# Kernel optimization log

Hardware: AMD Instinct MI355X
Metric: run time of the kernel (lower is better)

The kernel has to match this reference:

```python
import jax, jax.numpy as jnp
import numpy as np

B, S, HID = 1, 2048, 4096
H, HKV = 32, 8
D = HID // H          # 128
G = H // HKV          # 4 query heads per kv head (GQA)


def setup_inputs() -> dict:
    key = jax.random.key(0)
    ks = jax.random.split(key, 5)
    hidden_states = jax.random.normal(ks[0], (B, S, HID), dtype=jnp.float32)
    # additive causal mask: 0 on/below diagonal, large negative above
    causal = jnp.tril(jnp.ones((S, S), dtype=bool))
    attention_mask = jnp.where(causal, 0.0, -1e9).astype(jnp.float32)[None, None]
    sc = 0.02
    wq = jax.random.normal(ks[1], (HID, H * D), dtype=jnp.float32) * sc
    wk = jax.random.normal(ks[2], (HID, HKV * D), dtype=jnp.float32) * sc
    wv = jax.random.normal(ks[3], (HID, HKV * D), dtype=jnp.float32) * sc
    wo = jax.random.normal(ks[4], (H * D, HID), dtype=jnp.float32) * sc
    return {"hidden_states": hidden_states, "attention_mask": attention_mask,
            "wq": wq, "wk": wk, "wv": wv, "wo": wo}


def reference(hidden_states, attention_mask, wq, wk, wv, wo):
    # projections (lora_rank=0 path: plain dense, no bias)
    q = hidden_states @ wq                      # [B,S,H*D]
    k = hidden_states @ wk                      # [B,S,HKV*D]
    v = hidden_states @ wv                      # [B,S,HKV*D]
    # split heads; group query heads by their kv head: head h -> (h//G, h%G)
    q = q.reshape(B, S, HKV, G, D).transpose(0, 2, 3, 1, 4)   # [B,HKV,G,S,D]
    k = k.reshape(B, S, HKV, D).transpose(0, 2, 1, 3)          # [B,HKV,S,D]
    v = v.reshape(B, S, HKV, D).transpose(0, 2, 1, 3)          # [B,HKV,S,D]
    scale = 1.0 / jnp.sqrt(jnp.float32(D))
    # explicit S x S scores (as in source), with GQA kv broadcast over G
    scores = jnp.einsum('bkgsd,bktd->bkgst', q, k) * scale     # [B,HKV,G,S,S]
    scores = scores + attention_mask[:, :, None]               # broadcast over G
    probs = jax.nn.softmax(scores, axis=-1)
    attn = jnp.einsum('bkgst,bktd->bkgsd', probs, v)           # [B,HKV,G,S,D]
    attn = attn.transpose(0, 3, 1, 2, 4).reshape(B, S, H * D)  # [B,S,H*D]
    return attn @ wo                                           # [B,S,HID]
```

## Files before the change

kernel.cpp:

```cpp
#include <hip/hip_runtime.h>
#include <hip/hip_bf16.h>

#define S_LEN 2048
#define HID 4096
#define NH 32
#define NKV 8
#define HD 128
#define LDQKV 6144

typedef __bf16 bf16x8 __attribute__((ext_vector_type(8)));
typedef __bf16 bf16x4 __attribute__((ext_vector_type(4)));
typedef float f32x4 __attribute__((ext_vector_type(4)));

#define GLD16(gp, lp)                                                                   \
    __builtin_amdgcn_global_load_lds((const __attribute__((address_space(1))) void*)(gp), \
                                     (__attribute__((address_space(3))) void*)(lp), 16, 0, 0)

#define MFMA_BF16(a, b, c) __builtin_amdgcn_mfma_f32_16x16x32_bf16((a), (b), (c), 0, 0, 0)

__global__ void cast_bf16_kernel(const float* __restrict__ x, __bf16* __restrict__ y, int n) {
    int i = (blockIdx.x * blockDim.x + threadIdx.x) * 4;
    if (i < n) {
        float4 v = *reinterpret_cast<const float4*>(x + i);
        bf16x4 o;
        o.x = (__bf16)v.x; o.y = (__bf16)v.y; o.z = (__bf16)v.z; o.w = (__bf16)v.w;
        *reinterpret_cast<bf16x4*>(y + i) = o;
    }
}

__global__ void transpose_cast_kernel(const float* __restrict__ W, __bf16* __restrict__ WT,
                                      int K, int N, float scale) {
    __shared__ float tile[32][33];
    int bx = blockIdx.x;
    int by = blockIdx.y;
    int tx = threadIdx.x;
    int ty = threadIdx.y;
    int n = bx * 32 + tx;
#pragma unroll
    for (int i = 0; i < 4; i++) {
        int k = by * 32 + ty + i * 8;
        tile[ty + i * 8][tx] = W[(size_t)k * N + n];
    }
    __syncthreads();
    int k2 = by * 32 + tx;
#pragma unroll
    for (int i = 0; i < 4; i++) {
        int n2 = bx * 32 + ty + i * 8;
        WT[(size_t)n2 * K + k2] = (__bf16)(tile[tx][ty + i * 8] * scale);
    }
}

__global__ void transpose_bf16_kernel(const __bf16* __restrict__ V, int ldin,
                                      __bf16* __restrict__ VT, int ldout) {
    __shared__ __bf16 tile[32][33];
    int bx = blockIdx.x;
    int by = blockIdx.y;
    int tx = threadIdx.x;
    int ty = threadIdx.y;
#pragma unroll
    for (int i = 0; i < 4; i++)
        tile[ty + i * 8][tx] = V[(size_t)(by * 32 + ty + i * 8) * ldin + bx * 32 + tx];
    __syncthreads();
#pragma unroll
    for (int i = 0; i < 4; i++)
        VT[(size_t)(bx * 32 + ty + i * 8) * ldout + by * 32 + tx] = tile[tx][ty + i * 8];
}

template <int BM, typename OUT_T>
__global__ __launch_bounds__(512, 1) void gemm_pipe_kernel(const __bf16* __restrict__ A, int lda,
                                                           const __bf16* __restrict__ BT, int ldb,
                                                           OUT_T* __restrict__ C, int ldc, int K) {
    constexpr int MR = BM / 128;
    constexpr int AROUNDS = BM / 64;
    constexpr int NREADS = 4 * MR + 4;
    __shared__ __bf16 As[2][BM * 64];
    __shared__ __bf16 Bs[2][256 * 64];
    const int n0 = blockIdx.x * 256;
    const int m0 = blockIdx.y * BM;
    const int tid = threadIdx.x;
    const int lane = tid & 63, quad = lane >> 4, l16 = lane & 15;
    const int wave = tid >> 6;
    const int wg = (wave >> 2) * 64;
    const int wn32 = (wave & 3) * 32;

    f32x4 acc[4 * MR][4] = {};

    auto STAGE = [&](int b, int kb) {
#pragma unroll
        for (int r = 0; r < AROUNDS; r++) {
            int c = r * 512 + tid;
            int row = c >> 3;
            int col8 = (c & 7) ^ (row & 7);
            GLD16(&A[(size_t)(m0 + row) * lda + kb + col8 * 8], &As[b][c * 8]);
        }
#pragma unroll
        for (int r = 0; r < 4; r++) {
            int c = r * 512 + tid;
            int row = c >> 3;
            int col8 = (c & 7) ^ (row & 7);
            GLD16(&BT[(size_t)(n0 + row) * ldb + kb + col8 * 8], &Bs[b][c * 8]);
        }
    };

    auto READ_SET = [&](const __bf16* Asb, const __bf16* Bsb, int kk,
                        bf16x8 (&fa)[4 * MR], bf16x8 (&fb)[4]) {
        int slot = ((kk * 4 + quad) ^ (l16 & 7)) * 8;
#pragma unroll
        for (int i = 0; i < 4 * MR; i++) {
            int row = wg + (i & 3) * 16 + (i >> 2) * 128 + l16;
            fa[i] = *reinterpret_cast<const bf16x8*>(&Asb[row * 64 + slot]);
        }
#pragma unroll
        for (int j = 0; j < 4; j++) {
            int row = wn32 + (j & 1) * 16 + (j >> 1) * 128 + l16;
            fb[j] = *reinterpret_cast<const bf16x8*>(&Bsb[row * 64 + slot]);
        }
    };

    auto MF = [&](bf16x8 (&fa)[4 * MR], bf16x8 (&fb)[4]) {
        __builtin_amdgcn_s_setprio(1);
#pragma unroll
        for (int i = 0; i < 4 * MR; i++)
#pragma unroll
            for (int j = 0; j < 4; j++)
                acc[i][j] = MFMA_BF16(fa[i], fb[j], acc[i][j]);
        __builtin_amdgcn_s_setprio(0);
    };

    auto WAIT_SET = [&]() {
        if constexpr (NREADS == 12) {
            asm volatile("s_waitcnt lgkmcnt(12)" ::: "memory");
        } else {
            asm volatile("s_waitcnt lgkmcnt(8)" ::: "memory");
        }
        __builtin_amdgcn_sched_barrier(0);
    };

    const int nk = K >> 6;
    bf16x8 fa0[4 * MR], fb0[4], fa1[4 * MR], fb1[4];

    STAGE(0, 0);
    STAGE(1, 64);
    if constexpr (AROUNDS == 4) {
        asm volatile("s_waitcnt vmcnt(8)" ::: "memory");
    } else {
        asm volatile("s_waitcnt vmcnt(6)" ::: "memory");
    }
    __builtin_amdgcn_sched_barrier(0);
    __builtin_amdgcn_s_barrier();
    READ_SET(As[0], Bs[0], 0, fa0, fb0);

    for (int kt = 0; kt < nk; ++kt) {
        const int cur = kt & 1;
        READ_SET(As[cur], Bs[cur], 1, fa1, fb1);
        WAIT_SET();
        MF(fa0, fb0);
        if (kt + 1 < nk) {
            asm volatile("s_waitcnt vmcnt(0)" ::: "memory");
            __builtin_amdgcn_sched_barrier(0);
            __builtin_amdgcn_s_barrier();
            READ_SET(As[cur ^ 1], Bs[cur ^ 1], 0, fa0, fb0);
            WAIT_SET();
        } else {
            asm volatile("s_waitcnt lgkmcnt(0)" ::: "memory");
            __builtin_amdgcn_sched_barrier(0);
        }
        if (kt + 2 < nk) {
            __builtin_amdgcn_s_barrier();
            STAGE(cur, (kt + 2) << 6);
        }
        MF(fa1, fb1);
    }

#pragma unroll
    for (int i = 0; i < 4 * MR; i++)
#pragma unroll
        for (int j = 0; j < 4; j++)
#pragma unroll
            for (int r = 0; r < 4; r++) {
                int row = m0 + wg + (i & 3) * 16 + (i >> 2) * 128 + quad * 4 + r;
                int col = n0 + wn32 + (j & 1) * 16 + (j >> 1) * 128 + l16;
                C[(size_t)row * ldc + col] = (OUT_T)acc[i][j][r];
            }
}

__global__ __launch_bounds__(256) void attn_kernel(const __bf16* __restrict__ QKV,
                                                   const __bf16* __restrict__ VT,
                                                   __bf16* __restrict__ Ao,
                                                   __bf16* __restrict__ Opart,
                                                   float* __restrict__ Lp) {
    __shared__ __bf16 Ks[64 * 128];
    __shared__ __bf16 Vs[128 * 64];
    __shared__ __bf16 Pl[4][2][16 * 72];
    int x = blockIdx.x;
    int qt, c;
    if (x < 32) { qt = 31 - (x >> 1); c = x & 1; }
    else        { qt = 47 - x;        c = 0;     }
    int hp = blockIdx.y;
    int kvh = hp >> 1;
    int h0 = kvh * 4 + (hp & 1) * 2;
    int t0 = c ? 16 : 0;
    int t1 = c ? qt : min(qt, 15);
    int tid = threadIdx.x;
    int wave = tid >> 6, lane = tid & 63, quad = lane >> 4, l16 = lane & 15;
    int wq = qt * 64 + wave * 16;
    const __bf16* Kb = QKV + HID + (size_t)kvh * HD;
    const __bf16* Vt = VT + (size_t)kvh * HD * S_LEN;

    bf16x8 qf[2][4];
#pragma unroll
    for (int h = 0; h < 2; h++)
#pragma unroll
        for (int ks = 0; ks < 4; ks++)
            qf[h][ks] = *reinterpret_cast<const bf16x8*>(
                &QKV[(size_t)(wq + l16) * LDQKV + (h0 + h) * HD + ks * 32 + quad * 8]);

    bf16x8 ones;
#pragma unroll
    for (int j = 0; j < 8; j++) ones[j] = (__bf16)1.0f;

    f32x4 acc_o[2][8] = {};
    f32x4 lacc[2] = {};

    for (int t = t0; t <= t1; t++) {
        int kv0 = t << 6;
        bool diag = (t == qt);
        __syncthreads();
#pragma unroll
        for (int i = 0; i < 4; i++) {
            int cc = i * 256 + tid;
            int row = cc >> 4, sub = cc & 15;
            int col8 = sub ^ (row & 15);
            GLD16(&Kb[(size_t)(kv0 + row) * LDQKV + col8 * 8], &Ks[cc * 8]);
        }
#pragma unroll
        for (int i = 0; i < 4; i++) {
            int cc = i * 256 + tid;
            int row = cc >> 3, sub = cc & 7;
            int col8 = sub ^ (row & 7);
            GLD16(&Vt[(size_t)row * S_LEN + kv0 + col8 * 8], &Vs[cc * 8]);
        }
        __syncthreads();

        f32x4 sacc[2][4] = {};
#pragma unroll
        for (int ks = 0; ks < 4; ks++) {
            bf16x8 kf[4];
#pragma unroll
            for (int n = 0; n < 4; n++) {
                int row = n * 16 + l16;
                int sub = (ks * 4 + quad) ^ l16;
                kf[n] = *reinterpret_cast<const bf16x8*>(&Ks[row * 128 + sub * 8]);
            }
#pragma unroll
            for (int n = 0; n < 4; n++) {
                sacc[0][n] = MFMA_BF16(qf[0][ks], kf[n], sacc[0][n]);
                sacc[1][n] = MFMA_BF16(qf[1][ks], kf[n], sacc[1][n]);
            }
        }
#pragma unroll
        for (int h = 0; h < 2; h++) {
            __bf16* Pw = Pl[wave][h];
#pragma unroll
            for (int r = 0; r < 4; r++) {
                int row = wq + quad * 4 + r;
#pragma unroll
                for (int n = 0; n < 4; n++) {
                    float v = sacc[h][n][r];
                    if (diag) {
                        int col = kv0 + n * 16 + l16;
                        if (col > row) v = -1e30f;
                    }
                    Pw[(quad * 4 + r) * 72 + n * 16 + l16] =
                        (__bf16)__builtin_amdgcn_exp2f(v);
                }
            }
        }
#pragma unroll
        for (int ks = 0; ks < 2; ks++) {
            bf16x8 pf0 = *reinterpret_cast<const bf16x8*>(
                &Pl[wave][0][l16 * 72 + ks * 32 + quad * 8]);
            bf16x8 pf1 = *reinterpret_cast<const bf16x8*>(
                &Pl[wave][1][l16 * 72 + ks * 32 + quad * 8]);
            lacc[0] = MFMA_BF16(pf0, ones, lacc[0]);
            lacc[1] = MFMA_BF16(pf1, ones, lacc[1]);
#pragma unroll
            for (int dn = 0; dn < 8; dn++) {
                int row = dn * 16 + l16;
                int sub = (ks * 4 + quad) ^ (row & 7);
                bf16x8 vf = *reinterpret_cast<const bf16x8*>(&Vs[row * 64 + sub * 8]);
                acc_o[0][dn] = MFMA_BF16(pf0, vf, acc_o[0][dn]);
                acc_o[1][dn] = MFMA_BF16(pf1, vf, acc_o[1][dn]);
            }
        }
    }

    if (qt < 16) {
#pragma unroll
        for (int h = 0; h < 2; h++) {
            float rl[4];
#pragma unroll
            for (int r = 0; r < 4; r++) rl[r] = 1.0f / lacc[h][r];
#pragma unroll
            for (int dn = 0; dn < 8; dn++)
#pragma unroll
                for (int r = 0; r < 4; r++) {
                    int row = wq + quad * 4 + r;
                    int col = (h0 + h) * HD + dn * 16 + l16;
                    Ao[(size_t)row * HID + col] = (__bf16)(acc_o[h][dn][r] * rl[r]);
                }
        }
    } else {
        int s = (qt - 16) * 2 + c;
#pragma unroll
        for (int h = 0; h < 2; h++) {
            size_t base = ((size_t)(h0 + h) * 32 + s) * 64 + wave * 16;
#pragma unroll
            for (int dn = 0; dn < 8; dn++)
#pragma unroll
                for (int r = 0; r < 4; r++)
                    Opart[(base + quad * 4 + r) * 128 + dn * 16 + l16] =
                        (__bf16)acc_o[h][dn][r];
            if (l16 == 0) {
#pragma unroll
                for (int r = 0; r < 4; r++)
                    Lp[base + quad * 4 + r] = lacc[h][r];
            }
        }
    }
}

__global__ __launch_bounds__(256) void attn_combine(const __bf16* __restrict__ Opart,
                                                    const float* __restrict__ Lp,
                                                    __bf16* __restrict__ Ao) {
    int qt = 16 + (int)blockIdx.x;
    int h = blockIdx.y;
    int tid = threadIdx.x;
    size_t b0 = ((size_t)h * 32 + (qt - 16) * 2) * 64;
    size_t b1 = b0 + 64;
#pragma unroll 4
    for (int i = 0; i < 32; i++) {
        int el = i * 256 + tid;
        int rl = el >> 7, col = el & 127;
        float l = Lp[b0 + rl] + Lp[b1 + rl];
        float O = (float)Opart[(b0 + rl) * 128 + col] + (float)Opart[(b1 + rl) * 128 + col];
        int row = qt * 64 + rl;
        Ao[(size_t)row * HID + h * HD + col] = (__bf16)(O / l);
    }
}

extern "C" void kernel_launch(void* const* d_in, const int* in_sizes, int n_in,
                              void* d_out, int out_size, void* d_ws, size_t ws_size,
                              hipStream_t stream) {
    const float* hs = (const float*)d_in[0];
    const float* wq = (const float*)d_in[2];
    const float* wk = (const float*)d_in[3];
    const float* wv = (const float*)d_in[4];
    const float* wo = (const float*)d_in[5];
    float* out = (float*)d_out;

    char* ws = (char*)d_ws;
    __bf16* WqkvT = (__bf16*)(ws + (size_t)0);
    __bf16* Opart = (__bf16*)(ws + (size_t)0);
    float*  Lp    = (float*)(ws + ((size_t)20 << 20));
    __bf16* Xb    = (__bf16*)(ws + ((size_t)48 << 20));
    __bf16* QKV   = (__bf16*)(ws + ((size_t)64 << 20));
    __bf16* VTg   = (__bf16*)(ws + ((size_t)88 << 20));
    __bf16* Ab    = Xb;

    const int nX = S_LEN * HID;
    const float SC2 = 0.12751743f;

    cast_bf16_kernel<<<nX / 4 / 256, 256, 0, stream>>>(hs, Xb, nX);
    transpose_cast_kernel<<<dim3(128, 128), dim3(32, 8), 0, stream>>>(wq, WqkvT, HID, HID, SC2);
    transpose_cast_kernel<<<dim3(32, 128), dim3(32, 8), 0, stream>>>(
        wk, WqkvT + (size_t)4096 * HID, HID, NKV * HD, 1.0f);
    transpose_cast_kernel<<<dim3(32, 128), dim3(32, 8), 0, stream>>>(
        wv, WqkvT + (size_t)5120 * HID, HID, NKV * HD, 1.0f);
    gemm_pipe_kernel<256, __bf16><<<dim3(LDQKV / 256, S_LEN / 256), 512, 0, stream>>>(
        Xb, HID, WqkvT, HID, QKV, LDQKV, HID);
    transpose_bf16_kernel<<<dim3(32, 64), dim3(32, 8), 0, stream>>>(
        QKV + 5120, LDQKV, VTg, S_LEN);
    attn_kernel<<<dim3(48, 16), 256, 0, stream>>>(QKV, VTg, Ab, Opart, Lp);
    attn_combine<<<dim3(16, 32), 256, 0, stream>>>(Opart, Lp, Ab);
    transpose_cast_kernel<<<dim3(128, 128), dim3(32, 8), 0, stream>>>(wo, WqkvT, HID, HID, 1.0f);
    gemm_pipe_kernel<128, float><<<dim3(HID / 256, S_LEN / 128), 512, 0, stream>>>(
        Ab, HID, WqkvT, HID, out, HID, HID);
}
```

Measured before the change: 516.8 us.

## Switch GEMMs to 4-wave blocks with 2 blocks/CU and retuned tile shapes

```diff
diff --git a/kernel.cpp b/kernel.cpp
--- a/kernel.cpp
+++ b/kernel.cpp
@@ -66,36 +66,37 @@
         VT[(size_t)(bx * 32 + ty + i * 8) * ldout + by * 32 + tx] = tile[tx][ty + i * 8];
 }
 
-template <int BM, typename OUT_T>
-__global__ __launch_bounds__(512, 1) void gemm_pipe_kernel(const __bf16* __restrict__ A, int lda,
-                                                           const __bf16* __restrict__ BT, int ldb,
-                                                           OUT_T* __restrict__ C, int ldc, int K) {
-    constexpr int MR = BM / 128;
-    constexpr int AROUNDS = BM / 64;
-    constexpr int NREADS = 4 * MR + 4;
+template <int BM, int BN, typename OUT_T>
+__global__ __launch_bounds__(256, 2) void gemm_pipe2_kernel(const __bf16* __restrict__ A, int lda,
+                                                            const __bf16* __restrict__ BT, int ldb,
+                                                            OUT_T* __restrict__ C, int ldc, int K) {
+    constexpr int NFA = BM / 32;
+    constexpr int NFB = BN / 32;
+    constexpr int AR = BM / 32;
+    constexpr int BR = BN / 32;
     __shared__ __bf16 As[2][BM * 64];
-    __shared__ __bf16 Bs[2][256 * 64];
-    const int n0 = blockIdx.x * 256;
+    __shared__ __bf16 Bs[2][BN * 64];
+    const int n0 = blockIdx.x * BN;
     const int m0 = blockIdx.y * BM;
     const int tid = threadIdx.x;
     const int lane = tid & 63, quad = lane >> 4, l16 = lane & 15;
     const int wave = tid >> 6;
-    const int wg = (wave >> 2) * 64;
-    const int wn32 = (wave & 3) * 32;
-
-    f32x4 acc[4 * MR][4] = {};
+    const int wm = (wave >> 1) * (BM / 2);
+    const int wn = (wave & 1) * (BN / 2);
+
+    f32x4 acc[NFA][NFB] = {};
 
     auto STAGE = [&](int b, int kb) {
 #pragma unroll
-        for (int r = 0; r < AROUNDS; r++) {
-            int c = r * 512 + tid;
+        for (int r = 0; r < AR; r++) {
+            int c = r * 256 + tid;
             int row = c >> 3;
             int col8 = (c & 7) ^ (row & 7);
             GLD16(&A[(size_t)(m0 + row) * lda + kb + col8 * 8], &As[b][c * 8]);
         }
 #pragma unroll
-        for (int r = 0; r < 4; r++) {
-            int c = r * 512 + tid;
+        for (int r = 0; r < BR; r++) {
+            int c = r * 256 + tid;
             int row = c >> 3;
             int col8 = (c & 7) ^ (row & 7);
             GLD16(&BT[(size_t)(n0 + row) * ldb + kb + col8 * 8], &Bs[b][c * 8]);
@@ -103,48 +104,46 @@
     };
 
     auto READ_SET = [&](const __bf16* Asb, const __bf16* Bsb, int kk,
-                        bf16x8 (&fa)[4 * MR], bf16x8 (&fb)[4]) {
+                        bf16x8 (&fa)[NFA], bf16x8 (&fb)[NFB]) {
         int slot = ((kk * 4 + quad) ^ (l16 & 7)) * 8;
 #pragma unroll
-        for (int i = 0; i < 4 * MR; i++) {
-            int row = wg + (i & 3) * 16 + (i >> 2) * 128 + l16;
-            fa[i] = *reinterpret_cast<const bf16x8*>(&Asb[row * 64 + slot]);
-        }
-#pragma unroll
-        for (int j = 0; j < 4; j++) {
-            int row = wn32 + (j & 1) * 16 + (j >> 1) * 128 + l16;
-            fb[j] = *reinterpret_cast<const bf16x8*>(&Bsb[row * 64 + slot]);
-        }
+        for (int i = 0; i < NFA; i++)
+            fa[i] = *reinterpret_cast<const bf16x8*>(&Asb[(wm + i * 16 + l16) * 64 + slot]);
+#pragma unroll
+        for (int j = 0; j < NFB; j++)
+            fb[j] = *reinterpret_cast<const bf16x8*>(&Bsb[(wn + j * 16 + l16) * 64 + slot]);
     };
 
-    auto MF = [&](bf16x8 (&fa)[4 * MR], bf16x8 (&fb)[4]) {
+    auto MF = [&](bf16x8 (&fa)[NFA], bf16x8 (&fb)[NFB]) {
         __builtin_amdgcn_s_setprio(1);
 #pragma unroll
-        for (int i = 0; i < 4 * MR; i++)
-#pragma unroll
-            for (int j = 0; j < 4; j++)
+        for (int i = 0; i < NFA; i++)
+#pragma unroll
+            for (int j = 0; j < NFB; j++)
                 acc[i][j] = MFMA_BF16(fa[i], fb[j], acc[i][j]);
         __builtin_amdgcn_s_setprio(0);
     };
 
     auto WAIT_SET = [&]() {
-        if constexpr (NREADS == 12) {
+        if constexpr (NFA + NFB == 8) {
+            asm volatile("s_waitcnt lgkmcnt(8)" ::: "memory");
+        } else if constexpr (NFA + NFB == 10) {
+            asm volatile("s_waitcnt lgkmcnt(10)" ::: "memory");
+        } else {
             asm volatile("s_waitcnt lgkmcnt(12)" ::: "memory");
-        } else {
-            asm volatile("s_waitcnt lgkmcnt(8)" ::: "memory");
         }
         __builtin_amdgcn_sched_barrier(0);
     };
 
     const int nk = K >> 6;
-    bf16x8 fa0[4 * MR], fb0[4], fa1[4 * MR], fb1[4];
+    bf16x8 fa0[NFA], fb0[NFB], fa1[NFA], fb1[NFB];
 
     STAGE(0, 0);
     STAGE(1, 64);
-    if constexpr (AROUNDS == 4) {
+    if constexpr (AR + BR == 8) {
         asm volatile("s_waitcnt vmcnt(8)" ::: "memory");
     } else {
-        asm volatile("s_waitcnt vmcnt(6)" ::: "memory");
+        asm volatile("s_waitcnt vmcnt(10)" ::: "memory");
     }
     __builtin_amdgcn_sched_barrier(0);
     __builtin_amdgcn_s_barrier();
@@ -173,13 +172,13 @@
     }
 
 #pragma unroll
-    for (int i = 0; i < 4 * MR; i++)
-#pragma unroll
-        for (int j = 0; j < 4; j++)
+    for (int i = 0; i < NFA; i++)
+#pragma unroll
+        for (int j = 0; j < NFB; j++)
 #pragma unroll
             for (int r = 0; r < 4; r++) {
-                int row = m0 + wg + (i & 3) * 16 + (i >> 2) * 128 + quad * 4 + r;
-                int col = n0 + wn32 + (j & 1) * 16 + (j >> 1) * 128 + l16;
+                int row = m0 + wm + i * 16 + quad * 4 + r;
+                int col = n0 + wn + j * 16 + l16;
                 C[(size_t)row * ldc + col] = (OUT_T)acc[i][j][r];
             }
 }
@@ -377,13 +376,13 @@
         wk, WqkvT + (size_t)4096 * HID, HID, NKV * HD, 1.0f);
     transpose_cast_kernel<<<dim3(32, 128), dim3(32, 8), 0, stream>>>(
         wv, WqkvT + (size_t)5120 * HID, HID, NKV * HD, 1.0f);
-    gemm_pipe_kernel<256, __bf16><<<dim3(LDQKV / 256, S_LEN / 256), 512, 0, stream>>>(
+    gemm_pipe2_kernel<128, 192, __bf16><<<dim3(LDQKV / 192, S_LEN / 128), 256, 0, stream>>>(
         Xb, HID, WqkvT, HID, QKV, LDQKV, HID);
     transpose_bf16_kernel<<<dim3(32, 64), dim3(32, 8), 0, stream>>>(
         QKV + 5120, LDQKV, VTg, S_LEN);
     attn_kernel<<<dim3(48, 16), 256, 0, stream>>>(QKV, VTg, Ab, Opart, Lp);
     attn_combine<<<dim3(16, 32), 256, 0, stream>>>(Opart, Lp, Ab);
     transpose_cast_kernel<<<dim3(128, 128), dim3(32, 8), 0, stream>>>(wo, WqkvT, HID, HID, 1.0f);
-    gemm_pipe_kernel<128, float><<<dim3(HID / 256, S_LEN / 128), 512, 0, stream>>>(
+    gemm_pipe2_kernel<128, 128, float><<<dim3(HID / 128, S_LEN / 128), 256, 0, stream>>>(
         Ab, HID, WqkvT, HID, out, HID, HID);
 }
```

Measured after the change: 481.0 us. 1.07x faster.
